# Kernel tuning notes

Measured on AMD Instinct MI355X. Metric: run time of the kernel, lower is better.

Reference implementation:

```python
import jax, jax.numpy as jnp
import numpy as np

LATENT = 256

def setup_inputs() -> dict:
    key = jax.random.key(0)
    k1, k2, k3, k4, k5 = jax.random.split(key, 5)
    B, Te, Td, D = 4, 512, 256, LATENT
    encoder_output = jax.random.normal(k1, (B, Te, D), dtype=jnp.float32)
    decoder_output = jax.random.normal(k2, (B, Td, D), dtype=jnp.float32)
    # 'random_normal' keras initializer: stddev 0.05
    W_a = jax.random.normal(k3, (D, D), dtype=jnp.float32) * 0.05
    U_a = jax.random.normal(k4, (D, D), dtype=jnp.float32) * 0.05
    V_a = jax.random.normal(k5, (D, 1), dtype=jnp.float32) * 0.05
    return {"encoder_output": encoder_output, "decoder_output": decoder_output,
            "W_a": W_a, "U_a": U_a, "V_a": V_a}

def reference(encoder_output, decoder_output, W_a, U_a, V_a):
    # Projections computed once per position (mathematically equal to the
    # tiled tensordots in the original, without redundant GEMM work).
    W_enc = jnp.einsum('bed,df->bef', encoder_output, W_a)   # [B,Te,D]
    U_dec = jnp.einsum('btd,df->btf', decoder_output, U_a)   # [B,Td,D]
    # Broadcast add replaces the explicit tf.tile: [B,Td,Te,D]
    e = jnp.tanh(W_enc[:, None, :, :] + U_dec[:, :, None, :])
    score = jnp.einsum('bted,do->bte', e, V_a[:, 0:1])        # [B,Td,Te]
    attention_weights = jax.nn.softmax(score, axis=-1)
    context_vector = jnp.einsum('bte,bed->btd', attention_weights, encoder_output)
    return (context_vector, attention_weights)
```

## Files before the change

kernel.cpp:

```cpp
#include <hip/hip_runtime.h>

#define B 4
#define TE 512
#define TD 256
#define D 256

#define C2    2.8853900817779268f
#define LOG2E 1.4426950408889634f

__global__ __launch_bounds__(256) void proj_kernel(
    const float* __restrict__ enc, const float* __restrict__ dec,
    const float* __restrict__ Wa,  const float* __restrict__ Ua,
    float* __restrict__ ewt, float* __restrict__ eu)
{
    __shared__ float a_lds[8 * 256];
    const int tid = threadIdx.x;
    const int blk = blockIdx.x;
    const bool is_enc = blk < 256;
    const float* __restrict__ A = is_enc ? enc : dec;
    const float* __restrict__ W = is_enc ? Wa  : Ua;
    const int row0 = (is_enc ? blk : blk - 256) * 8;

    {
        const float4* src = (const float4*)(A + (size_t)row0 * 256);
        ((float4*)a_lds)[tid]       = src[tid];
        ((float4*)a_lds)[tid + 256] = src[tid + 256];
    }
    __syncthreads();

    float acc[8] = {0.f,0.f,0.f,0.f,0.f,0.f,0.f,0.f};

    #pragma unroll 4
    for (int k = 0; k < 256; k += 4) {
        const float w0 = W[(k + 0) * 256 + tid];
        const float w1 = W[(k + 1) * 256 + tid];
        const float w2 = W[(k + 2) * 256 + tid];
        const float w3 = W[(k + 3) * 256 + tid];
        #pragma unroll
        for (int r = 0; r < 8; r++) {
            const float4 a4 = *(const float4*)&a_lds[r * 256 + k];
            acc[r] = fmaf(a4.x, w0, acc[r]);
            acc[r] = fmaf(a4.y, w1, acc[r]);
            acc[r] = fmaf(a4.z, w2, acc[r]);
            acc[r] = fmaf(a4.w, w3, acc[r]);
        }
    }

    float f[8];
    #pragma unroll
    for (int r = 0; r < 8; r++)
        f[r] = __builtin_amdgcn_exp2f(acc[r] * C2);

    if (is_enc) {
        const int b  = row0 >> 9;
        const int e0 = row0 & 511;
        float* o = ewt + ((size_t)(b * 256 + tid)) * 512 + e0;
        *(float4*)(o + 0) = make_float4(f[0], f[1], f[2], f[3]);
        *(float4*)(o + 4) = make_float4(f[4], f[5], f[6], f[7]);
    } else {
        #pragma unroll
        for (int r = 0; r < 8; r++)
            eu[(row0 + r) * 256 + tid] = f[r];
    }
}

__device__ __forceinline__ void qcomb4(float& q, const float4& v,
                                       float p0, float p1, float p2, float p3)
{
    const float n01 = fmaf(v.y, p0, v.x * p1);
    const float d01 = p0 * p1;
    const float n23 = fmaf(v.w, p2, v.z * p3);
    const float d23 = p2 * p3;
    const float num = fmaf(n23, d01, n01 * d23);
    const float den = d01 * d23;
    q = fmaf(num, __builtin_amdgcn_rcpf(den), q);
}

__global__ __launch_bounds__(1024) void attn_kernel(
    const float* __restrict__ enc, const float* __restrict__ ewt,
    const float* __restrict__ eu,  const float* __restrict__ Va,
    float* __restrict__ ctx, float* __restrict__ aw)
{
    __shared__ float eul[4 * 256];
    __shared__ float val[256];
    __shared__ float sc[4][TE];
    __shared__ float wred[2][4][4];
    __shared__ float part[4][4][256];

    const int tid = threadIdx.x;
    const int b   = blockIdx.x >> 6;
    const int t0  = (blockIdx.x & 63) * 4;
    const int bt0 = b * 256 + t0;

    if (tid < 256) val[tid] = Va[tid];
    eul[tid] = eu[(size_t)bt0 * 256 + tid];
    __syncthreads();

    {
        const int e  = tid & 511;
        const int tp = tid >> 9;
        const float* __restrict__ ewb = ewt + (size_t)b * 256 * 512 + e;
        const float* __restrict__ ea0 = &eul[(2 * tp + 0) * 256];
        const float* __restrict__ ea1 = &eul[(2 * tp + 1) * 256];

        float q0 = 0.f, q1 = 0.f;

        for (int d = 0; d < 256; d += 8) {
            float w[8];
            #pragma unroll
            for (int j = 0; j < 8; j++) w[j] = ewb[(d + j) * 512];

            #pragma unroll
            for (int h = 0; h < 2; h++) {
                const int dd = d + h * 4;
                const float4 v4 = *(const float4*)&val[dd];
                const float4 a0 = *(const float4*)&ea0[dd];
                const float4 a1 = *(const float4*)&ea1[dd];
                const float* wj = &w[h * 4];

                qcomb4(q0, v4,
                       fmaf(wj[0], a0.x, 1.0f), fmaf(wj[1], a0.y, 1.0f),
                       fmaf(wj[2], a0.z, 1.0f), fmaf(wj[3], a0.w, 1.0f));
                qcomb4(q1, v4,
                       fmaf(wj[0], a1.x, 1.0f), fmaf(wj[1], a1.y, 1.0f),
                       fmaf(wj[2], a1.z, 1.0f), fmaf(wj[3], a1.w, 1.0f));
            }
        }
        sc[2 * tp + 0][e] = -2.0f * q0;
        sc[2 * tp + 1][e] = -2.0f * q1;
    }
    __syncthreads();

    {
        const int wv   = tid >> 6;
        const int lane = tid & 63;
        const int t    = wv >> 2;
        const int seg  = wv & 3;
        float* __restrict__ srow = &sc[t][seg * 128];

        const float x0 = srow[lane];
        const float x1 = srow[lane + 64];

        float m = fmaxf(x0, x1);
        #pragma unroll
        for (int s = 32; s > 0; s >>= 1) m = fmaxf(m, __shfl_xor(m, s, 64));
        if (lane == 0) wred[0][t][seg] = m;
        __syncthreads();
        const float4 mm = *(const float4*)&wred[0][t][0];
        const float M = fmaxf(fmaxf(mm.x, mm.y), fmaxf(mm.z, mm.w));

        const float g0 = __builtin_amdgcn_exp2f((x0 - M) * LOG2E);
        const float g1 = __builtin_amdgcn_exp2f((x1 - M) * LOG2E);

        float ssum = g0 + g1;
        #pragma unroll
        for (int s = 32; s > 0; s >>= 1) ssum += __shfl_xor(ssum, s, 64);
        if (lane == 0) wred[1][t][seg] = ssum;
        __syncthreads();
        const float4 sm = *(const float4*)&wred[1][t][0];
        const float inv = __builtin_amdgcn_rcpf((sm.x + sm.y) + (sm.z + sm.w));

        const float p0 = g0 * inv, p1 = g1 * inv;
        srow[lane]      = p0;
        srow[lane + 64] = p1;
        float* __restrict__ ao = aw + ((size_t)(bt0 + t)) * 512 + seg * 128;
        ao[lane]      = p0;
        ao[lane + 64] = p1;
    }
    __syncthreads();

    {
        const int eg = tid >> 8;
        const int dl = tid & 255;
        const float* __restrict__ eb =
            enc + ((size_t)b * 512 + eg * 128) * 256 + dl;
        const int e0 = eg * 128;

        float c0 = 0.f, c1 = 0.f, c2 = 0.f, c3 = 0.f;
        #pragma unroll 4
        for (int j = 0; j < 128; j += 4) {
            const float4 w0 = *(const float4*)&sc[0][e0 + j];
            const float4 w1 = *(const float4*)&sc[1][e0 + j];
            const float4 w2 = *(const float4*)&sc[2][e0 + j];
            const float4 w3 = *(const float4*)&sc[3][e0 + j];
            const float r0 = eb[(j + 0) * 256];
            const float r1 = eb[(j + 1) * 256];
            const float r2 = eb[(j + 2) * 256];
            const float r3 = eb[(j + 3) * 256];
            c0 = fmaf(w0.x, r0, c0); c0 = fmaf(w0.y, r1, c0); c0 = fmaf(w0.z, r2, c0); c0 = fmaf(w0.w, r3, c0);
            c1 = fmaf(w1.x, r0, c1); c1 = fmaf(w1.y, r1, c1); c1 = fmaf(w1.z, r2, c1); c1 = fmaf(w1.w, r3, c1);
            c2 = fmaf(w2.x, r0, c2); c2 = fmaf(w2.y, r1, c2); c2 = fmaf(w2.z, r2, c2); c2 = fmaf(w2.w, r3, c2);
            c3 = fmaf(w3.x, r0, c3); c3 = fmaf(w3.y, r1, c3); c3 = fmaf(w3.z, r2, c3); c3 = fmaf(w3.w, r3, c3);
        }
        part[eg][0][dl] = c0;
        part[eg][1][dl] = c1;
        part[eg][2][dl] = c2;
        part[eg][3][dl] = c3;
    }
    __syncthreads();

    {
        const int t  = tid >> 8;
        const int dl = tid & 255;
        ctx[((size_t)(bt0 + t)) * 256 + dl] =
            (part[0][t][dl] + part[1][t][dl]) +
            (part[2][t][dl] + part[3][t][dl]);
    }
}

extern "C" void kernel_launch(void* const* d_in, const int* in_sizes, int n_in,
                              void* d_out, int out_size, void* d_ws, size_t ws_size,
                              hipStream_t stream) {
    const float* enc = (const float*)d_in[0];
    const float* dec = (const float*)d_in[1];
    const float* Wa  = (const float*)d_in[2];
    const float* Ua  = (const float*)d_in[3];
    const float* Va  = (const float*)d_in[4];

    float* out = (float*)d_out;
    float* ctx = out;
    float* aw  = out + B * TD * D;

    float* ewt = (float*)d_ws;
    float* eu  = ewt + (size_t)B * D * TE;

    proj_kernel<<<dim3(384), dim3(256), 0, stream>>>(enc, dec, Wa, Ua, ewt, eu);
    attn_kernel<<<dim3(256), dim3(1024), 0, stream>>>(enc, ewt, eu, Va, ctx, aw);
}
```

Before: 106.0 us.

## Fuse decoder projection into attention kernel, interleave ewt layout, XCD-aware block mapping

```diff
diff --git a/kernel.cpp b/kernel.cpp
--- a/kernel.cpp
+++ b/kernel.cpp
@@ -8,21 +8,39 @@
 #define C2    2.8853900817779268f
 #define LOG2E 1.4426950408889634f
 
+__device__ __forceinline__ void qcomb4(float& q, const float4& v,
+                                       float p0, float p1, float p2, float p3)
+{
+    const float n01 = fmaf(v.y, p0, v.x * p1);
+    const float d01 = p0 * p1;
+    const float n23 = fmaf(v.w, p2, v.z * p3);
+    const float d23 = p2 * p3;
+    const float num = fmaf(n23, d01, n01 * d23);
+    const float den = d01 * d23;
+    q = fmaf(num, __builtin_amdgcn_rcpf(den), q);
+}
+
+__device__ __forceinline__ void score4(float& q, const float4& v4,
+                                       const float4& w, const float4& a)
+{
+    qcomb4(q, v4, fmaf(w.x, a.x, 1.0f), fmaf(w.y, a.y, 1.0f),
+                  fmaf(w.z, a.z, 1.0f), fmaf(w.w, a.w, 1.0f));
+}
+
 __global__ __launch_bounds__(256) void proj_kernel(
-    const float* __restrict__ enc, const float* __restrict__ dec,
-    const float* __restrict__ Wa,  const float* __restrict__ Ua,
-    float* __restrict__ ewt, float* __restrict__ eu)
+    const float* __restrict__ enc, const float* __restrict__ Wa,
+    float* __restrict__ ewt)
 {
     __shared__ float a_lds[8 * 256];
     const int tid = threadIdx.x;
     const int blk = blockIdx.x;
-    const bool is_enc = blk < 256;
-    const float* __restrict__ A = is_enc ? enc : dec;
-    const float* __restrict__ W = is_enc ? Wa  : Ua;
-    const int row0 = (is_enc ? blk : blk - 256) * 8;
-
-    {
-        const float4* src = (const float4*)(A + (size_t)row0 * 256);
+    const int xcd = blk & 7;
+    const int b   = xcd >> 1;
+    const int j   = ((xcd & 1) << 5) | (blk >> 3);
+    const int e0  = j * 8;
+
+    {
+        const float4* src = (const float4*)(enc + ((size_t)(b * 512 + e0)) * 256);
         ((float4*)a_lds)[tid]       = src[tid];
         ((float4*)a_lds)[tid + 256] = src[tid + 256];
     }
@@ -32,10 +50,10 @@
 
     #pragma unroll 4
     for (int k = 0; k < 256; k += 4) {
-        const float w0 = W[(k + 0) * 256 + tid];
-        const float w1 = W[(k + 1) * 256 + tid];
-        const float w2 = W[(k + 2) * 256 + tid];
-        const float w3 = W[(k + 3) * 256 + tid];
+        const float w0 = Wa[(k + 0) * 256 + tid];
+        const float w1 = Wa[(k + 1) * 256 + tid];
+        const float w2 = Wa[(k + 2) * 256 + tid];
+        const float w3 = Wa[(k + 3) * 256 + tid];
         #pragma unroll
         for (int r = 0; r < 8; r++) {
             const float4 a4 = *(const float4*)&a_lds[r * 256 + k];
@@ -46,88 +64,108 @@
         }
     }
 
-    float f[8];
+    float* o = ewt + (((size_t)(b * 64 + (tid >> 2)) * 512 + e0) << 2) + (tid & 3);
     #pragma unroll
     for (int r = 0; r < 8; r++)
-        f[r] = __builtin_amdgcn_exp2f(acc[r] * C2);
-
-    if (is_enc) {
-        const int b  = row0 >> 9;
-        const int e0 = row0 & 511;
-        float* o = ewt + ((size_t)(b * 256 + tid)) * 512 + e0;
-        *(float4*)(o + 0) = make_float4(f[0], f[1], f[2], f[3]);
-        *(float4*)(o + 4) = make_float4(f[4], f[5], f[6], f[7]);
-    } else {
-        #pragma unroll
-        for (int r = 0; r < 8; r++)
-            eu[(row0 + r) * 256 + tid] = f[r];
-    }
-}
-
-__device__ __forceinline__ void qcomb4(float& q, const float4& v,
-                                       float p0, float p1, float p2, float p3)
-{
-    const float n01 = fmaf(v.y, p0, v.x * p1);
-    const float d01 = p0 * p1;
-    const float n23 = fmaf(v.w, p2, v.z * p3);
-    const float d23 = p2 * p3;
-    const float num = fmaf(n23, d01, n01 * d23);
-    const float den = d01 * d23;
-    q = fmaf(num, __builtin_amdgcn_rcpf(den), q);
+        o[r * 4] = __builtin_amdgcn_exp2f(acc[r] * C2);
 }
 
 __global__ __launch_bounds__(1024) void attn_kernel(
-    const float* __restrict__ enc, const float* __restrict__ ewt,
-    const float* __restrict__ eu,  const float* __restrict__ Va,
+    const float* __restrict__ enc, const float* __restrict__ dec,
+    const float* __restrict__ Ua,  const float* __restrict__ Va,
+    const float* __restrict__ ewt,
     float* __restrict__ ctx, float* __restrict__ aw)
 {
     __shared__ float eul[4 * 256];
     __shared__ float val[256];
+    __shared__ float decl[4 * 256];
     __shared__ float sc[4][TE];
     __shared__ float wred[2][4][4];
     __shared__ float part[4][4][256];
 
     const int tid = threadIdx.x;
-    const int b   = blockIdx.x >> 6;
-    const int t0  = (blockIdx.x & 63) * 4;
+    const int blk = blockIdx.x;
+    const int xcd = blk & 7;
+    const int b   = xcd >> 1;
+    const int tq  = ((xcd & 1) << 5) | (blk >> 3);
+    const int t0  = tq * 4;
     const int bt0 = b * 256 + t0;
 
+    float* const scratch = &part[0][0][0];
+
     if (tid < 256) val[tid] = Va[tid];
-    eul[tid] = eu[(size_t)bt0 * 256 + tid];
+    decl[tid] = dec[(size_t)bt0 * 256 + tid];
+    __syncthreads();
+
+    {
+        const int dg = tid & 63;
+        const int t  = (tid >> 6) & 3;
+        const int kq = tid >> 8;
+        const float4* Ua4 = (const float4*)Ua;
+        const float*  dr  = &decl[t * 256];
+        float4 a4 = make_float4(0.f, 0.f, 0.f, 0.f);
+        #pragma unroll 4
+        for (int i = 0; i < 64; ++i) {
+            const int k = kq * 64 + i;
+            const float  dv = dr[k];
+            const float4 u4 = Ua4[k * 64 + dg];
+            a4.x = fmaf(dv, u4.x, a4.x);
+            a4.y = fmaf(dv, u4.y, a4.y);
+            a4.z = fmaf(dv, u4.z, a4.z);
+            a4.w = fmaf(dv, u4.w, a4.w);
+        }
+        ((float4*)scratch)[(kq * 4 + t) * 64 + dg] = a4;
+    }
+    __syncthreads();
+    {
+        const float s = scratch[tid] + scratch[1024 + tid] +
+                        scratch[2048 + tid] + scratch[3072 + tid];
+        eul[tid] = __builtin_amdgcn_exp2f(s * C2);
+    }
     __syncthreads();
 
     {
         const int e  = tid & 511;
         const int tp = tid >> 9;
-        const float* __restrict__ ewb = ewt + (size_t)b * 256 * 512 + e;
-        const float* __restrict__ ea0 = &eul[(2 * tp + 0) * 256];
-        const float* __restrict__ ea1 = &eul[(2 * tp + 1) * 256];
-
-        float q0 = 0.f, q1 = 0.f;
-
-        for (int d = 0; d < 256; d += 8) {
-            float w[8];
-            #pragma unroll
-            for (int j = 0; j < 8; j++) w[j] = ewb[(d + j) * 512];
-
-            #pragma unroll
-            for (int h = 0; h < 2; h++) {
-                const int dd = d + h * 4;
-                const float4 v4 = *(const float4*)&val[dd];
-                const float4 a0 = *(const float4*)&ea0[dd];
-                const float4 a1 = *(const float4*)&ea1[dd];
-                const float* wj = &w[h * 4];
-
-                qcomb4(q0, v4,
-                       fmaf(wj[0], a0.x, 1.0f), fmaf(wj[1], a0.y, 1.0f),
-                       fmaf(wj[2], a0.z, 1.0f), fmaf(wj[3], a0.w, 1.0f));
-                qcomb4(q1, v4,
-                       fmaf(wj[0], a1.x, 1.0f), fmaf(wj[1], a1.y, 1.0f),
-                       fmaf(wj[2], a1.z, 1.0f), fmaf(wj[3], a1.w, 1.0f));
+        const float4* __restrict__ ewb =
+            (const float4*)ewt + (size_t)(b * 64 + tp * 32) * 512 + e;
+        float q0 = 0.f, q1 = 0.f, q2 = 0.f, q3 = 0.f;
+
+        #pragma unroll 2
+        for (int it = 0; it < 16; ++it) {
+            const float4 w0 = ewb[(it * 2 + 0) * 512];
+            const float4 w1 = ewb[(it * 2 + 1) * 512];
+            const int d0 = (tp * 32 + it * 2) * 4;
+            {
+                const float4 v4 = *(const float4*)&val[d0];
+                score4(q0, v4, w0, *(const float4*)&eul[      d0]);
+                score4(q1, v4, w0, *(const float4*)&eul[256 + d0]);
+                score4(q2, v4, w0, *(const float4*)&eul[512 + d0]);
+                score4(q3, v4, w0, *(const float4*)&eul[768 + d0]);
             }
-        }
-        sc[2 * tp + 0][e] = -2.0f * q0;
-        sc[2 * tp + 1][e] = -2.0f * q1;
+            {
+                const int d1 = d0 + 4;
+                const float4 v4 = *(const float4*)&val[d1];
+                score4(q0, v4, w1, *(const float4*)&eul[      d1]);
+                score4(q1, v4, w1, *(const float4*)&eul[256 + d1]);
+                score4(q2, v4, w1, *(const float4*)&eul[512 + d1]);
+                score4(q3, v4, w1, *(const float4*)&eul[768 + d1]);
+            }
+        }
+
+        if (tp) {
+            scratch[       e] = q0;
+            scratch[512  + e] = q1;
+            scratch[1024 + e] = q2;
+            scratch[1536 + e] = q3;
+        }
+        __syncthreads();
+        if (!tp) {
+            sc[0][e] = -2.0f * (q0 + scratch[       e]);
+            sc[1][e] = -2.0f * (q1 + scratch[512  + e]);
+            sc[2][e] = -2.0f * (q2 + scratch[1024 + e]);
+            sc[3][e] = -2.0f * (q3 + scratch[1536 + e]);
+        }
     }
     __syncthreads();
 
@@ -178,15 +216,15 @@
 
         float c0 = 0.f, c1 = 0.f, c2 = 0.f, c3 = 0.f;
         #pragma unroll 4
-        for (int j = 0; j < 128; j += 4) {
-            const float4 w0 = *(const float4*)&sc[0][e0 + j];
-            const float4 w1 = *(const float4*)&sc[1][e0 + j];
-            const float4 w2 = *(const float4*)&sc[2][e0 + j];
-            const float4 w3 = *(const float4*)&sc[3][e0 + j];
-            const float r0 = eb[(j + 0) * 256];
-            const float r1 = eb[(j + 1) * 256];
-            const float r2 = eb[(j + 2) * 256];
-            const float r3 = eb[(j + 3) * 256];
+        for (int jj = 0; jj < 128; jj += 4) {
+            const float4 w0 = *(const float4*)&sc[0][e0 + jj];
+            const float4 w1 = *(const float4*)&sc[1][e0 + jj];
+            const float4 w2 = *(const float4*)&sc[2][e0 + jj];
+            const float4 w3 = *(const float4*)&sc[3][e0 + jj];
+            const float r0 = eb[(jj + 0) * 256];
+            const float r1 = eb[(jj + 1) * 256];
+            const float r2 = eb[(jj + 2) * 256];
+            const float r3 = eb[(jj + 3) * 256];
             c0 = fmaf(w0.x, r0, c0); c0 = fmaf(w0.y, r1, c0); c0 = fmaf(w0.z, r2, c0); c0 = fmaf(w0.w, r3, c0);
             c1 = fmaf(w1.x, r0, c1); c1 = fmaf(w1.y, r1, c1); c1 = fmaf(w1.z, r2, c1); c1 = fmaf(w1.w, r3, c1);
             c2 = fmaf(w2.x, r0, c2); c2 = fmaf(w2.y, r1, c2); c2 = fmaf(w2.z, r2, c2); c2 = fmaf(w2.w, r3, c2);
@@ -222,8 +260,7 @@
     float* aw  = out + B * TD * D;
 
     float* ewt = (float*)d_ws;
-    float* eu  = ewt + (size_t)B * D * TE;
-
-    proj_kernel<<<dim3(384), dim3(256), 0, stream>>>(enc, dec, Wa, Ua, ewt, eu);
-    attn_kernel<<<dim3(256), dim3(1024), 0, stream>>>(enc, ewt, eu, Va, ctx, aw);
-}
+
+    proj_kernel<<<dim3(256), dim3(256),  0, stream>>>(enc, Wa, ewt);
+    attn_kernel<<<dim3(256), dim3(1024), 0, stream>>>(enc, dec, Ua, Va, ewt, ctx, aw);
+}
```

New measurement: 110.7 us. 1.04x slower.
